# Performance work log

Measured on AMD Instinct MI355X. Metric: run time of the kernel, lower is better.

Reference implementation:

```python
import jax, jax.numpy as jnp
import numpy as np

B, S, D, H, HD = 4, 2048, 768, 12, 64
P = H * HD
LR = 0.1

def _ln(x, g, b, eps=1e-5):
    m = jnp.mean(x, axis=-1, keepdims=True)
    v = jnp.mean((x - m) ** 2, axis=-1, keepdims=True)
    return (x - m) / jnp.sqrt(v + eps) * g + b

def _modifier(x, w1, b1, w2, b2):
    # Linear -> GELU(exact) -> Linear, matching nn.Sequential(Linear, GELU, Linear)
    h = jax.nn.gelu(x @ w1.T + b1, approximate=False)
    return h @ w2.T + b2

def setup_inputs() -> dict:
    key = jax.random.key(0)
    ks = jax.random.split(key, 16)
    def n(k, shape, s=0.02):
        return jax.random.normal(k, shape, jnp.float32) * s
    inp = {}
    inp['x'] = jax.random.normal(ks[0], (B, S, D), jnp.float32)
    inp['ln_in_g'] = jnp.ones((D,), jnp.float32)
    inp['ln_in_b'] = jnp.zeros((D,), jnp.float32)
    inp['Wk'] = n(ks[1], (P, D))
    inp['Wv'] = n(ks[2], (P, D))
    inp['Wq'] = n(ks[3], (P, D))
    inp['km_w1'] = n(ks[4], (D // 4, D), 0.01); inp['km_b1'] = jnp.zeros((D // 4,), jnp.float32)
    inp['km_w2'] = n(ks[5], (P, D // 4), 0.01); inp['km_b2'] = jnp.zeros((P,), jnp.float32)
    inp['vm_w1'] = n(ks[6], (D // 4, D), 0.01); inp['vm_b1'] = jnp.zeros((D // 4,), jnp.float32)
    inp['vm_w2'] = n(ks[7], (P, D // 4), 0.01); inp['vm_b2'] = jnp.zeros((P,), jnp.float32)
    inp['qm_w1'] = n(ks[8], (D // 4, D), 0.01); inp['qm_b1'] = jnp.zeros((D // 4,), jnp.float32)
    inp['qm_w2'] = n(ks[9], (P, D // 4), 0.01); inp['qm_b2'] = jnp.zeros((P,), jnp.float32)
    inp['lnk_g'] = jnp.ones((HD,), jnp.float32); inp['lnk_b'] = jnp.zeros((HD,), jnp.float32)
    inp['lnv_g'] = jnp.ones((HD,), jnp.float32); inp['lnv_b'] = jnp.zeros((HD,), jnp.float32)
    inp['lnq_g'] = jnp.ones((HD,), jnp.float32); inp['lnq_b'] = jnp.zeros((HD,), jnp.float32)
    inp['Wo'] = n(ks[10], (D, P))
    inp['lr_scale'] = jnp.ones((H,), jnp.float32)
    inp['Wg'] = n(ks[11], (D, D))
    inp['bg'] = jnp.zeros((D,), jnp.float32)
    return inp

def reference(x, ln_in_g, ln_in_b, Wk, Wv, Wq,
              km_w1, km_b1, km_w2, km_b2,
              vm_w1, vm_b1, vm_w2, vm_b2,
              qm_w1, qm_b1, qm_w2, qm_b2,
              lnk_g, lnk_b, lnv_g, lnv_b, lnq_g, lnq_b,
              Wo, lr_scale, Wg, bg):
    b, s, d = x.shape
    xn = _ln(x, ln_in_g, ln_in_b)  # norm_input
    # data-dependent projections (context defaults to x_normed)
    k = xn @ Wk.T + 0.1 * _modifier(xn, km_w1, km_b1, km_w2, km_b2)
    v = xn @ Wv.T + 0.1 * _modifier(xn, vm_w1, vm_b1, vm_w2, vm_b2)
    q = xn @ Wq.T + 0.1 * _modifier(xn, qm_w1, qm_b1, qm_w2, qm_b2)
    k = _ln(k.reshape(b, s, H, HD), lnk_g, lnk_b)
    v = _ln(v.reshape(b, s, H, HD), lnv_g, lnv_b)
    q = _ln(q.reshape(b, s, H, HD), lnq_g, lnq_b)
    # scan over time: (s, b, h, d)
    k_s = jnp.transpose(k, (1, 0, 2, 3))
    v_s = jnp.transpose(v, (1, 0, 2, 3))
    q_s = jnp.transpose(q, (1, 0, 2, 3))
    lr = jax.nn.sigmoid(lr_scale) * LR * 2.0  # (H,)
    M0 = jnp.zeros((b, H, HD, HD), x.dtype)

    def step(M, kvq):
        k_t, v_t, q_t = kvq  # each (b, h, d)
        out_t = jnp.einsum('bhdk,bhk->bhd', M, q_t)  # read before update
        kn = k_t / (jnp.linalg.norm(k_t, axis=-1, keepdims=True) + 1e-6)
        pred = jnp.einsum('bhdk,bhk->bhd', M, kn)
        surprise = pred - v_t
        # M - outer(pred, kn) - lr * outer(surprise, kn), fused
        coef = pred + lr[None, :, None] * surprise  # (b, h, d)
        M_new = M - jnp.einsum('bhd,bhk->bhdk', coef, kn)
        return M_new, out_t

    M_final, outs = jax.lax.scan(step, M0, (k_s, v_s, q_s))  # outs: (s, b, h, d)
    out = jnp.transpose(outs, (1, 0, 2, 3)).reshape(b, s, H * HD)
    out = out @ Wo.T
    gate = jax.nn.sigmoid(x @ Wg.T + bg)  # output_gate on raw x
    out = gate * out
    return out, M_final
```

## Files before the change

kernel.cpp:

```cpp
#include <hip/hip_runtime.h>
#include <hip/hip_bf16.h>
#include <math.h>

#define B_ 4
#define S_ 2048
#define D_ 768
#define H_ 12
#define HD_ 64
#define P_ 768
#define M_ (B_*S_)
#define NCH 32
#define CH 64
#define BH (B_*H_)
#define NPAIR 16

typedef __hip_bfloat16 bf16;
typedef __attribute__((ext_vector_type(8))) short short8;
typedef __attribute__((ext_vector_type(4))) short s16x4;
typedef __attribute__((ext_vector_type(4))) float f32x4;

__device__ __forceinline__ float wave_reduce_sum(float v){
  #pragma unroll
  for (int off=32; off>0; off>>=1) v += __shfl_xor(v, off, 64);
  return v;
}
__device__ __forceinline__ float bf2f(bf16 h){ return __bfloat162float(h); }
__device__ __forceinline__ float us2f(unsigned short u){
  union{unsigned int i; float f;} z; z.i = ((unsigned int)u)<<16; return z.f;
}
__device__ __forceinline__ int adr(int row, int col){ return (row*128 + col*2) ^ ((row&7)<<4); }
__device__ __forceinline__ short8 lfrag(const char* base, int row, int col){
  return *(const short8*)(base + adr(row,col));
}
__device__ __forceinline__ short8 gfrag(const bf16* g, int row, int col){
  return *(const short8*)(g + row*64 + col);
}
__device__ __forceinline__ f32x4 MM(short8 a, short8 b, f32x4 c){
  return __builtin_amdgcn_mfma_f32_16x16x32_bf16(a, b, c, 0,0,0);
}
__device__ __forceinline__ short f2s(float v){ bf16 h = __float2bfloat16(v); return *(short*)&h; }
__device__ __forceinline__ void stpk(char* b, int n, int m0, float v0,float v1,float v2,float v3){
  s16x4 p = { f2s(v0), f2s(v1), f2s(v2), f2s(v3) };
  *(s16x4*)(b + adr(n, m0)) = p;
}
__device__ __forceinline__ void stpk_hl(char* bh, char* bl, int n, int m0,
                                        float v0,float v1,float v2,float v3){
  float h0=bf2f(__float2bfloat16(v0)), h1=bf2f(__float2bfloat16(v1));
  float h2=bf2f(__float2bfloat16(v2)), h3=bf2f(__float2bfloat16(v3));
  stpk(bh, n, m0, h0,h1,h2,h3);
  stpk(bl, n, m0, v0-h0, v1-h1, v2-h2, v3-h3);
}
__device__ __forceinline__ float4 ldpk2(const char* bh, const char* bl, int n, int m0){
  s16x4 a = *(const s16x4*)(bh + adr(n,m0));
  s16x4 b = *(const s16x4*)(bl + adr(n,m0));
  return make_float4(us2f((unsigned short)a[0])+us2f((unsigned short)b[0]),
                     us2f((unsigned short)a[1])+us2f((unsigned short)b[1]),
                     us2f((unsigned short)a[2])+us2f((unsigned short)b[2]),
                     us2f((unsigned short)a[3])+us2f((unsigned short)b[3]));
}
__device__ __forceinline__ void gl_lds(const bf16* g, const bf16* l){
  __builtin_amdgcn_global_load_lds(
      (const __attribute__((address_space(1))) void*)g,
      (__attribute__((address_space(3))) void*)l, 16, 0, 0);
}

__global__ __launch_bounds__(256) void pack_ln_kernel(
    const float* __restrict__ km1,const float* __restrict__ vm1,const float* __restrict__ qm1,
    const float* __restrict__ Wk,const float* __restrict__ Wv,const float* __restrict__ Wq,
    const float* __restrict__ k2,const float* __restrict__ v2,const float* __restrict__ q2,
    const float* __restrict__ Wo,const float* __restrict__ Wg,
    const float* __restrict__ kb1,const float* __restrict__ vb1,const float* __restrict__ qb1,
    const float* __restrict__ kb2,const float* __restrict__ vb2,const float* __restrict__ qb2,
    const float* __restrict__ lnkg,const float* __restrict__ lnvg,const float* __restrict__ lnqg,
    const float* __restrict__ lnkb,const float* __restrict__ lnvb,const float* __restrict__ lnqb,
    bf16* __restrict__ Whb, bf16* __restrict__ Wkvqb, bf16* __restrict__ Wob,
    bf16* __restrict__ Wgb, float* __restrict__ biasb,
    const float* __restrict__ x, const float* __restrict__ lng_in, const float* __restrict__ lnb_in,
    bf16* __restrict__ xn, bf16* __restrict__ xb)
{
  if (blockIdx.x >= 15181){
    int row = blockIdx.x - 15181;
    const float* xr = x + (size_t)row*D_;
    int t = threadIdx.x;
    float v0 = xr[t], v1 = xr[t+256], v2 = xr[t+512];
    float s  = v0+v1+v2;
    float sq = v0*v0+v1*v1+v2*v2;
    s = wave_reduce_sum(s); sq = wave_reduce_sum(sq);
    __shared__ float red[8];
    int w = t>>6;
    if ((t&63)==0){ red[w]=s; red[4+w]=sq; }
    __syncthreads();
    s  = red[0]+red[1]+red[2]+red[3];
    sq = red[4]+red[5]+red[6]+red[7];
    float mean = s*(1.f/D_);
    float var  = sq*(1.f/D_) - mean*mean;
    float inv  = rsqrtf(var + 1e-5f);
    bf16* xnr = xn + (size_t)row*D_;
    bf16* xbr = xb + (size_t)row*D_;
    xnr[t]     = __float2bfloat16((v0-mean)*inv*lng_in[t]     + lnb_in[t]);
    xnr[t+256] = __float2bfloat16((v1-mean)*inv*lng_in[t+256] + lnb_in[t+256]);
    xnr[t+512] = __float2bfloat16((v2-mean)*inv*lng_in[t+512] + lnb_in[t+512]);
    xbr[t] = __float2bfloat16(v0); xbr[t+256] = __float2bfloat16(v1); xbr[t+512] = __float2bfloat16(v2);
    return;
  }
  int i = blockIdx.x*256 + threadIdx.x;
  if (i < 491520){
    int r = i/768, c = i%768;
    float v = 0.f;
    if (r < 192) v = km1[r*768+c];
    else if (r < 384) v = vm1[(r-192)*768+c];
    else if (r < 576) v = qm1[(r-384)*768+c];
    Whb[i] = __float2bfloat16(v);
  } else if (i < 2703360){
    int i2 = i - 491520;
    int r = i2/960, c = i2%960;
    int p = r/768, rr = r%768;
    const float* W  = (p==0)?Wk:(p==1)?Wv:Wq;
    const float* w2 = (p==0)?k2:(p==1)?v2:q2;
    float v = (c < 768) ? W[(size_t)rr*768+c] : 0.1f*w2[(size_t)rr*192 + (c-768)];
    Wkvqb[i2] = __float2bfloat16(v);
  } else if (i < 3293184){
    int i2 = i - 2703360;
    Wob[i2] = __float2bfloat16(Wo[i2]);
  } else if (i < 3883008){
    int i2 = i - 3293184;
    Wgb[i2] = __float2bfloat16(Wg[i2]);
  } else if (i < 3886272){
    int i2 = i - 3883008;
    if (i2 < 576){
      biasb[i2] = (i2<192)? kb1[i2] : (i2<384)? vb1[i2-192] : qb1[i2-384];
    } else if (i2 < 2880){
      int r = i2-576; int p = r/768, rr = r%768;
      const float* b2 = (p==0)?kb2:(p==1)?vb2:qb2;
      biasb[i2] = 0.1f*b2[rr];
    } else if (i2 < 3072){
      int k3 = i2-2880; int gg=k3/64, cc=k3%64;
      biasb[i2] = (gg==0?lnkg:gg==1?lnvg:lnqg)[cc];
    } else {
      int k3 = i2-3072; int gg=k3/64, cc=k3%64;
      biasb[i2] = (gg==0?lnkb:gg==1?lnvb:lnqb)[cc];
    }
  }
}

template<int MODE>
__device__ __forceinline__ void gemm_core(
    const bf16* __restrict__ A1, int lda1, int K1,
    const bf16* __restrict__ A2, int lda2, int K2, int a2_gstride,
    const bf16* __restrict__ Bw, int ldb, int ngroup,
    const float* __restrict__ bias, const void* __restrict__ extra,
    const float* __restrict__ lng, const float* __restrict__ lnb,
    void* __restrict__ outp, int Nout,
    int bx, int by, int g, char* smemraw)
{
  bf16 (*Asm)[128*32] = (bf16 (*)[128*32])smemraw;
  bf16 (*Bsm)[128*32] = (bf16 (*)[128*32])(smemraw + 3*128*32*2);
  const int t = threadIdx.x;
  const int w = t>>6, L = t&63;
  const int m0 = bx*128, n0 = by*128;
  const int wm = w>>1, wn = w&1;
  const int Ktot = K1 + K2;
  const int nk = Ktot >> 5;

  const int srow = L>>2;
  const int scol8 = ((L&3) ^ ((L>>2)&3))*8;

  int aoff[4], boff[4];
  #pragma unroll
  for (int f=0;f<4;f++){
    int arow = wm*64 + f*16 + (L&15);
    int brow = wn*64 + f*16 + (L&15);
    aoff[f] = arow*32 + (((L>>4) ^ (arow&3))<<3);
    boff[f] = brow*32 + (((L>>4) ^ (brow&3))<<3);
  }

  const bf16* BrowBase = Bw + (size_t)(g*ngroup + n0)*ldb;

  auto STAGE = [&](int buf, int k0){
    const bf16* Ab; int lda; int acol;
    if (k0 < K1){ Ab = A1; lda = lda1; acol = k0 + scol8; }
    else        { Ab = A2; lda = lda2; acol = (k0-K1) + g*a2_gstride + scol8; }
    #pragma unroll
    for (int i=0;i<2;i++){
      int row = w*32 + i*16 + srow;
      gl_lds(Ab + (size_t)(m0+row)*lda + acol,         &Asm[buf][w*1024 + i*512]);
      gl_lds(BrowBase + (size_t)row*ldb + k0 + scol8,  &Bsm[buf][w*1024 + i*512]);
    }
  };

  f32x4 acc[4][4];
  #pragma unroll
  for (int i=0;i<4;i++)
    #pragma unroll
    for (int j=0;j<4;j++) acc[i][j] = (f32x4){0.f,0.f,0.f,0.f};

  STAGE(0, 0);
  STAGE(1, 32);
  int rd = 0;
  for (int kt=0; kt<nk; ++kt){
    if (kt == nk-1) asm volatile("s_waitcnt vmcnt(0)" ::: "memory");
    else            asm volatile("s_waitcnt vmcnt(4)" ::: "memory");
    asm volatile("s_waitcnt lgkmcnt(0)" ::: "memory");
    __builtin_amdgcn_s_barrier();
    __builtin_amdgcn_sched_barrier(0);
    if (kt+2 < nk){
      int st = rd+2; if (st>=3) st-=3;
      STAGE(st, (kt+2)<<5);
    }
    const bf16* As = Asm[rd];
    const bf16* Bs = Bsm[rd];
    short8 af[4], bfr[4];
    #pragma unroll
    for (int f=0;f<4;f++){
      af[f]  = *(const short8*)&As[aoff[f]];
      bfr[f] = *(const short8*)&Bs[boff[f]];
    }
    #pragma unroll
    for (int i=0;i<4;i++)
      #pragma unroll
      for (int j=0;j<4;j++)
        acc[i][j] = MM(af[i], bfr[j], acc[i][j]);
    rd = (rd==2)?0:rd+1;
  }

  if (MODE==1){
    float gco[4], bco[4];
    #pragma unroll
    for (int j=0;j<4;j++){ int cc = j*16 + (L&15); gco[j] = lng[g*64+cc]; bco[j] = lnb[g*64+cc]; }
    #pragma unroll
    for (int i=0;i<4;i++){
      #pragma unroll
      for (int r=0;r<4;r++){
        float v[4];
        #pragma unroll
        for (int j=0;j<4;j++){
          int n = n0 + wn*64 + j*16 + (L&15);
          v[j] = acc[i][j][r] + bias[g*768 + n];
        }
        float s1 = v[0]+v[1]+v[2]+v[3];
        float s2 = v[0]*v[0]+v[1]*v[1]+v[2]*v[2]+v[3]*v[3];
        #pragma unroll
        for (int mk=1; mk<16; mk<<=1){ s1 += __shfl_xor(s1, mk, 64); s2 += __shfl_xor(s2, mk, 64); }
        float mean = s1*(1.f/64.f);
        float var  = s2*(1.f/64.f) - mean*mean;
        float inv  = rsqrtf(var + 1e-5f);
        float y[4];
        #pragma unroll
        for (int j=0;j<4;j++) y[j] = (v[j]-mean)*inv*gco[j] + bco[j];
        if (g==0){
          float n2 = y[0]*y[0]+y[1]*y[1]+y[2]*y[2]+y[3]*y[3];
          #pragma unroll
          for (int mk=1; mk<16; mk<<=1) n2 += __shfl_xor(n2, mk, 64);
          float sc = 1.f/(sqrtf(n2)+1e-6f);
          #pragma unroll
          for (int j=0;j<4;j++) y[j] *= sc;
        }
        int m = m0 + wm*64 + i*16 + (L>>4)*4 + r;
        int b_ = m>>11, s_ = m&2047;
        #pragma unroll
        for (int j=0;j<4;j++){
          int n = n0 + wn*64 + j*16 + (L&15);
          int h_ = n>>6, hd = n&63;
          ((bf16*)outp)[((((size_t)g*B_ + b_)*H_ + h_)*S_ + s_)*HD_ + hd] = __float2bfloat16(y[j]);
        }
      }
    }
  } else {
    #pragma unroll
    for (int i=0;i<4;i++){
      #pragma unroll
      for (int j=0;j<4;j++){
        #pragma unroll
        for (int r=0;r<4;r++){
          int m = m0 + wm*64 + i*16 + (L>>4)*4 + r;
          int n = n0 + wn*64 + j*16 + (L&15);
          float val = acc[i][j][r];
          if (MODE==0){
            if (n < Nout){
              val += bias[n];
              float ge = 0.5f*val*(1.f + erff(val*0.70710678f));
              ((bf16*)outp)[(size_t)m*Nout + n] = __float2bfloat16(ge);
            }
          } else if (MODE==4){
            ((bf16*)outp)[(size_t)m*Nout + n] = __float2bfloat16(val);
          } else {
            float g2 = bf2f(((const bf16*)extra)[(size_t)m*768 + n]) + bias[n];
            float gate = 1.f/(1.f + __expf(-g2));
            ((float*)outp)[(size_t)m*Nout + n] = val * gate;
          }
        }
      }
    }
  }
}

template<int MODE>
__global__ __launch_bounds__(256) void gemm_kernel(
    const bf16* __restrict__ A1, int lda1, int K1,
    const bf16* __restrict__ A2, int lda2, int K2, int a2_gstride,
    const bf16* __restrict__ Bw, int ldb, int ngroup,
    const float* __restrict__ bias, const void* __restrict__ extra,
    const float* __restrict__ lng, const float* __restrict__ lnb,
    void* __restrict__ outp, int Nout)
{
  __shared__ __align__(16) char smem[49152];
  gemm_core<MODE>(A1, lda1, K1, A2, lda2, K2, a2_gstride, Bw, ldb, ngroup,
                  bias, extra, lng, lnb, outp, Nout,
                  blockIdx.x, blockIdx.y, blockIdx.z, smem);
}

__global__ __launch_bounds__(256) void prep_kernel(
    const bf16* __restrict__ kvqb, const float* __restrict__ lr_scale,
    bf16* __restrict__ WKng, bf16* __restrict__ WVTg,
    bf16* __restrict__ AcThi, bf16* __restrict__ AcTlo, bf16* __restrict__ Bcb)
{
  __shared__ __align__(16) char T1[8192];
  __shared__ __align__(16) char T2[8192];
  __shared__ __align__(16) char T3[8192];
  __shared__ __align__(16) char T4[8192];
  __shared__ __align__(16) char T5[8192];

  const int c = blockIdx.x, bh = blockIdx.y;
  const int h = bh % H_;
  const int t = threadIdx.x, w = t>>6, L = t&63;
  const size_t PS = (size_t)B_*H_*S_*HD_;
  const size_t base_k = (size_t)bh*S_*HD_ + (size_t)c*CH*HD_;
  const float lr = 0.2f/(1.f + __expf(-lr_scale[h]));
  const float beta = 1.f + lr;
  const size_t cb = ((size_t)bh*NCH + c)*4096;
  const bf16* Kg = kvqb + base_k;
  const bf16* Vg = kvqb + PS + base_k;

  const int fr = L&15, fc = (L>>4)*8;
  const int m0 = 16*w + (L>>4)*4;
  const int nb = L&15;

  {
    short8 aK[2];
    #pragma unroll
    for (int kk=0;kk<2;kk++) aK[kk] = gfrag(Kg, 16*w+fr, kk*32+fc);
    #pragma unroll
    for (int nt=0;nt<4;nt++){
      f32x4 g = (f32x4){0.f,0.f,0.f,0.f};
      #pragma unroll
      for (int kk=0;kk<2;kk++) g = MM(aK[kk], gfrag(Kg, 16*nt+fr, kk*32+fc), g);
      int n = 16*nt + nb;
      float pv[4], ptv[4], tv[4];
      #pragma unroll
      for (int r=0;r<4;r++){
        int m = m0 + r;
        float val = beta*g[r];
        pv[r]  = (n>m)? val : 0.f;
        ptv[r] = (m>n)? val : 0.f;
        tv[r]  = ((n==m)?1.f:0.f) - pv[r];
      }
      stpk(T3, n, m0, pv[0],pv[1],pv[2],pv[3]);
      stpk(T4, n, m0, ptv[0],ptv[1],ptv[2],ptv[3]);
      stpk_hl(T1, T2, n, m0, tv[0],tv[1],tv[2],tv[3]);
    }
  }
  __syncthreads();

  #pragma unroll
  for (int s=0; s<6; ++s){
    const bool do_upd = (s>=1), do_sq = (s<=4);
    f32x4 upd[4], c1[4], c2[4];
    float4 tr[4];
    short8 aPT[2];
    #pragma unroll
    for (int kk=0;kk<2;kk++) aPT[kk] = lfrag(T4, 16*w+fr, kk*32+fc);
    if (do_upd){
      short8 b1[4][2], b2[4][2];
      #pragma unroll
      for (int nt=0;nt<4;nt++){
        #pragma unroll
        for (int kk=0;kk<2;kk++){
          b1[nt][kk] = lfrag(T1, 16*nt+fr, kk*32+fc);
          b2[nt][kk] = lfrag(T2, 16*nt+fr, kk*32+fc);
        }
        upd[nt] = (f32x4){0.f,0.f,0.f,0.f};
      }
      #pragma unroll
      for (int nt=0;nt<4;nt++)
        #pragma unroll
        for (int kk=0;kk<2;kk++){
          upd[nt] = MM(aPT[kk], b1[nt][kk], upd[nt]);
          upd[nt] = MM(aPT[kk], b2[nt][kk], upd[nt]);
        }
      #pragma unroll
      for (int nt=0;nt<4;nt++) tr[nt] = ldpk2(T1, T2, 16*nt+nb, m0);
    }
    if (do_sq){
      short8 aP[2], bPT[4][2], bP[4][2];
      #pragma unroll
      for (int kk=0;kk<2;kk++) aP[kk] = lfrag(T3, 16*w+fr, kk*32+fc);
      #pragma unroll
      for (int nt=0;nt<4;nt++){
        #pragma unroll
        for (int kk=0;kk<2;kk++){
          bPT[nt][kk] = lfrag(T4, 16*nt+fr, kk*32+fc);
          bP[nt][kk]  = lfrag(T3, 16*nt+fr, kk*32+fc);
        }
        c1[nt] = (f32x4){0.f,0.f,0.f,0.f};
        c2[nt] = (f32x4){0.f,0.f,0.f,0.f};
      }
      #pragma unroll
      for (int nt=0;nt<4;nt++)
        #pragma unroll
        for (int kk=0;kk<2;kk++){
          c1[nt] = MM(aP[kk],  bPT[nt][kk], c1[nt]);
          c2[nt] = MM(aPT[kk], bP[nt][kk],  c2[nt]);
        }
    }
    __syncthreads();
    if (do_upd){
      #pragma unroll
      for (int nt=0;nt<4;nt++){
        int n = 16*nt + nb;
        stpk_hl(T1, T2, n, m0, tr[nt].x+upd[nt][0], tr[nt].y+upd[nt][1],
                               tr[nt].z+upd[nt][2], tr[nt].w+upd[nt][3]);
      }
    }
    if (do_sq){
      #pragma unroll
      for (int nt=0;nt<4;nt++){
        int n = 16*nt + nb;
        stpk(T4, n, m0, c1[nt][0],c1[nt][1],c1[nt][2],c1[nt][3]);
        stpk(T3, n, m0, c2[nt][0],c2[nt][1],c2[nt][2],c2[nt][3]);
      }
    }
    __syncthreads();
  }

  {
    short8 aKg[2], aVg[2];
    #pragma unroll
    for (int kk=0;kk<2;kk++){
      aKg[kk] = gfrag(Kg, 16*w+fr, kk*32+fc);
      aVg[kk] = gfrag(Vg, 16*w+fr, kk*32+fc);
    }
    #pragma unroll
    for (int nt=0;nt<4;nt++){
      f32x4 ck = (f32x4){0.f,0.f,0.f,0.f};
      f32x4 cv = (f32x4){0.f,0.f,0.f,0.f};
      int row = 16*nt + nb;
      #pragma unroll
      for (int kk=0;kk<2;kk++){
        short8 bi;
        int col0 = kk*32 + fc;
        #pragma unroll
        for (int e=0;e<8;e++) bi[e] = (col0+e == 16*nt+fr) ? (short)0x3F80 : (short)0;
        ck = MM(aKg[kk], bi, ck);
        cv = MM(aVg[kk], bi, cv);
      }
      stpk(T3, row, m0, ck[0],ck[1],ck[2],ck[3]);
      stpk(T4, row, m0, cv[0],cv[1],cv[2],cv[3]);
    }
  }
  __syncthreads();

  {
    short8 a1[2], a2[2];
    #pragma unroll
    for (int kk=0;kk<2;kk++){
      a1[kk] = lfrag(T1, 16*w+fr, kk*32+fc);
      a2[kk] = lfrag(T2, 16*w+fr, kk*32+fc);
    }
    f32x4 cwv[4], cwk[4];
    #pragma unroll
    for (int nt=0;nt<4;nt++){ cwv[nt]=(f32x4){0.f,0.f,0.f,0.f}; cwk[nt]=(f32x4){0.f,0.f,0.f,0.f}; }
    #pragma unroll
    for (int nt=0;nt<4;nt++)
      #pragma unroll
      for (int kk=0;kk<2;kk++){
        short8 bV = lfrag(T4, 16*nt+fr, kk*32+fc);
        cwv[nt] = MM(a1[kk], bV, cwv[nt]);
        cwv[nt] = MM(a2[kk], bV, cwv[nt]);
      }
    #pragma unroll
    for (int nt=0;nt<4;nt++)
      #pragma unroll
      for (int kk=0;kk<2;kk++){
        short8 bK = lfrag(T3, 16*nt+fr, kk*32+fc);
        cwk[nt] = MM(a1[kk], bK, cwk[nt]);
        cwk[nt] = MM(a2[kk], bK, cwk[nt]);
      }
    __syncthreads();
    #pragma unroll
    for (int nt=0;nt<4;nt++){
      int n = 16*nt + nb;
      stpk(T5, n, m0, cwv[nt][0],cwv[nt][1],cwv[nt][2],cwv[nt][3]);
      stpk(T4, n, m0, cwk[nt][0],cwk[nt][1],cwk[nt][2],cwk[nt][3]);
    }
  }
  __syncthreads();

  {
    int row = t>>2, seg = (t&3)*16;
    size_t go = cb + (size_t)row*64 + seg;
    *(short8*)(WVTg+go)   = *(const short8*)(T5 + adr(row,seg));
    *(short8*)(WVTg+go+8) = *(const short8*)(T5 + adr(row,seg+8));

    short8 aK2[2], aWKT[2];
    #pragma unroll
    for (int kk=0;kk<2;kk++){
      aK2[kk]  = lfrag(T3, 16*w+fr, kk*32+fc);
      aWKT[kk] = lfrag(T4, 16*w+fr, kk*32+fc);
    }
    f32x4 cBc[4], cWK[4], cAc[4];
    #pragma unroll
    for (int nt=0;nt<4;nt++){ cBc[nt]=(f32x4){0.f,0.f,0.f,0.f}; cWK[nt]=(f32x4){0.f,0.f,0.f,0.f}; cAc[nt]=(f32x4){0.f,0.f,0.f,0.f}; }
    #pragma unroll
    for (int nt=0;nt<4;nt++)
      #pragma unroll
      for (int kk=0;kk<2;kk++){
        short8 bWVT = lfrag(T5, 16*nt+fr, kk*32+fc);
        cBc[nt] = MM(aK2[kk], bWVT, cBc[nt]);
      }
    #pragma unroll
    for (int nt=0;nt<4;nt++)
      #pragma unroll
      for (int kk=0;kk<2;kk++){
        short8 b1 = lfrag(T1, 16*nt+fr, kk*32+fc);
        short8 b2 = lfrag(T2, 16*nt+fr, kk*32+fc);
        cWK[nt] = MM(aK2[kk], b1, cWK[nt]);
        cWK[nt] = MM(aK2[kk], b2, cWK[nt]);
      }
    #pragma unroll
    for (int nt=0;nt<4;nt++)
      #pragma unroll
      for (int kk=0;kk<2;kk++){
        short8 bK3 = lfrag(T3, 16*nt+fr, kk*32+fc);
        cAc[nt] = MM(aWKT[kk], bK3, cAc[nt]);
      }
    __syncthreads();
    #pragma unroll
    for (int nt=0;nt<4;nt++){
      int n = 16*nt + nb;
      stpk(T5, n, m0, lr*cBc[nt][0], lr*cBc[nt][1], lr*cBc[nt][2], lr*cBc[nt][3]);
      stpk(T3, n, m0, cWK[nt][0],cWK[nt][1],cWK[nt][2],cWK[nt][3]);
      float av[4];
      #pragma unroll
      for (int r=0;r<4;r++) av[r] = ((n==m0+r)?1.f:0.f) - beta*cAc[nt][r];
      stpk_hl(T1, T2, n, m0, av[0],av[1],av[2],av[3]);
    }
  }
  __syncthreads();

  {
    int row = t>>2, seg = (t&3)*16;
    size_t go = cb + (size_t)row*64 + seg;
    *(short8*)(AcThi+go)   = *(const short8*)(T1 + adr(row,seg));
    *(short8*)(AcThi+go+8) = *(const short8*)(T1 + adr(row,seg+8));
    *(short8*)(AcTlo+go)   = *(const short8*)(T2 + adr(row,seg));
    *(short8*)(AcTlo+go+8) = *(const short8*)(T2 + adr(row,seg+8));
    *(short8*)(Bcb+go)     = *(const short8*)(T5 + adr(row,seg));
    *(short8*)(Bcb+go+8)   = *(const short8*)(T5 + adr(row,seg+8));
    *(short8*)(WKng+go)    = *(const short8*)(T3 + adr(row,seg));
    *(short8*)(WKng+go+8)  = *(const short8*)(T3 + adr(row,seg+8));
  }
}

__global__ __launch_bounds__(256) void prep2_kernel(
    const bf16* __restrict__ AcThi, const bf16* __restrict__ AcTlo, const bf16* __restrict__ Bcb,
    bf16* __restrict__ A2h, bf16* __restrict__ A2l,
    bf16* __restrict__ BT2h, bf16* __restrict__ BT2l)
{
  __shared__ __align__(16) char TA[8192];
  __shared__ __align__(16) char TB[8192];
  const int i = blockIdx.x, bh = blockIdx.y;
  const int t = threadIdx.x, w = t>>6, L = t&63;
  const size_t cb0 = ((size_t)bh*NCH + 2*i)*4096;
  const size_t cb1 = cb0 + 4096;
  const size_t pb  = ((size_t)bh*NPAIR + i)*4096;
  const int fr = L&15, fc = (L>>4)*8;
  const int m0 = 16*w + (L>>4)*4;
  const int nb = L&15;

  {
    short8 s0[2], s1[2];
    #pragma unroll
    for (int kk=0;kk<2;kk++){
      s0[kk] = *(const short8*)(AcThi + cb0 + (size_t)(16*w+fr)*64 + kk*32 + fc);
      s1[kk] = *(const short8*)(AcTlo + cb0 + (size_t)(16*w+fr)*64 + kk*32 + fc);
    }
    #pragma unroll
    for (int nt=0;nt<4;nt++){
      f32x4 c0v={0.f,0.f,0.f,0.f}, c1v={0.f,0.f,0.f,0.f};
      #pragma unroll
      for (int kk=0;kk<2;kk++){
        short8 bi;
        int col0 = kk*32 + fc;
        #pragma unroll
        for (int e=0;e<8;e++) bi[e] = (col0+e == 16*nt+fr) ? (short)0x3F80 : (short)0;
        c0v = MM(s0[kk], bi, c0v);
        c1v = MM(s1[kk], bi, c1v);
      }
      stpk(TA, 16*nt+nb, m0, c0v[0],c0v[1],c0v[2],c0v[3]);
      stpk(TB, 16*nt+nb, m0, c1v[0],c1v[1],c1v[2],c1v[3]);
    }
  }
  __syncthreads();
  {
    short8 aTh[2], aTl[2], gAh[2], gAl[2];
    #pragma unroll
    for (int kk=0;kk<2;kk++){
      aTh[kk] = lfrag(TA, 16*w+fr, kk*32+fc);
      aTl[kk] = lfrag(TB, 16*w+fr, kk*32+fc);
      gAh[kk] = *(const short8*)(AcThi + cb1 + (size_t)(16*w+fr)*64 + kk*32 + fc);
      gAl[kk] = *(const short8*)(AcTlo + cb1 + (size_t)(16*w+fr)*64 + kk*32 + fc);
    }
    #pragma unroll
    for (int nt=0;nt<4;nt++){
      short8 gBh[2], gBl[2], bB0[2];
      #pragma unroll
      for (int kk=0;kk<2;kk++){
        gBh[kk] = *(const short8*)(AcThi + cb1 + (size_t)(16*nt+fr)*64 + kk*32 + fc);
        gBl[kk] = *(const short8*)(AcTlo + cb1 + (size_t)(16*nt+fr)*64 + kk*32 + fc);
        bB0[kk] = *(const short8*)(Bcb   + cb0 + (size_t)(16*nt+fr)*64 + kk*32 + fc);
      }
      f32x4 accA = {0.f,0.f,0.f,0.f};
      s16x4 b1pk = *(const s16x4*)(Bcb + cb1 + (size_t)(16*nt+nb)*64 + m0);
      f32x4 accB = { us2f((unsigned short)b1pk[0]), us2f((unsigned short)b1pk[1]),
                     us2f((unsigned short)b1pk[2]), us2f((unsigned short)b1pk[3]) };
      #pragma unroll
      for (int kk=0;kk<2;kk++){
        accA = MM(aTh[kk], gBh[kk], accA);
        accA = MM(aTl[kk], gBh[kk], accA);
        accA = MM(aTh[kk], gBl[kk], accA);
        accB = MM(gAh[kk], bB0[kk], accB);
        accB = MM(gAl[kk], bB0[kk], accB);
      }
      int n = 16*nt + nb;
      size_t go = pb + (size_t)n*64 + m0;
      float h0[4], l0[4], h1[4], l1[4];
      #pragma unroll
      for (int r=0;r<4;r++){
        h0[r] = bf2f(__float2bfloat16(accA[r])); l0[r] = accA[r]-h0[r];
        h1[r] = bf2f(__float2bfloat16(accB[r])); l1[r] = accB[r]-h1[r];
      }
      s16x4 pa = { f2s(h0[0]), f2s(h0[1]), f2s(h0[2]), f2s(h0[3]) };
      s16x4 pbv= { f2s(l0[0]), f2s(l0[1]), f2s(l0[2]), f2s(l0[3]) };
      s16x4 pc = { f2s(h1[0]), f2s(h1[1]), f2s(h1[2]), f2s(h1[3]) };
      s16x4 pd = { f2s(l1[0]), f2s(l1[1]), f2s(l1[2]), f2s(l1[3]) };
      *(s16x4*)(A2h  + go) = pa;
      *(s16x4*)(A2l  + go) = pbv;
      *(s16x4*)(BT2h + go) = pc;
      *(s16x4*)(BT2l + go) = pd;
    }
  }
}

__global__ __launch_bounds__(256) void seq_kernel(
    const bf16* __restrict__ AcThi, const bf16* __restrict__ AcTlo, const bf16* __restrict__ Bcb,
    const bf16* __restrict__ A2h, const bf16* __restrict__ A2l,
    const bf16* __restrict__ BT2h, const bf16* __restrict__ BT2l,
    bf16* __restrict__ Mpref, bf16* __restrict__ Mplo, float* __restrict__ Mout,
    const bf16* __restrict__ xb, const bf16* __restrict__ Wgb, bf16* __restrict__ G2b)
{
  __shared__ __align__(16) char smem[49152];
  if (blockIdx.x >= BH){
    int bidx = blockIdx.x - BH;
    gemm_core<4>(xb, 768, 768, nullptr, 0, 0, 0, Wgb, 768, 768,
                 nullptr, nullptr, nullptr, nullptr, G2b, 768,
                 bidx & 63, bidx >> 6, 0, smem);
    return;
  }
  char* sH0 = smem;           char* sH1 = smem + 8192;
  char* sL0 = smem + 16384;   char* sL1 = smem + 24576;
  const int bh = blockIdx.x;
  const int t = threadIdx.x, w = t>>6, L = t&63;
  const size_t cbase = (size_t)bh*NCH*4096;
  const size_t pbase = (size_t)bh*NPAIR*4096;
  const int fr = L&15, fc = (L>>4)*8;
  const int nb = L&15, cmr = (L>>4)*4;
  const int m0 = 16*w + cmr;

  { float4 z = {0.f,0.f,0.f,0.f};
    ((float4*)sH0)[t] = z; ((float4*)sH0)[t+256] = z;
    ((float4*)sL0)[t] = z; ((float4*)sL0)[t+256] = z;
    short8 zs = {0,0,0,0,0,0,0,0};
    ((short8*)(Mpref + cbase))[t] = zs; ((short8*)(Mpref + cbase))[t+256] = zs;
    ((short8*)(Mplo  + cbase))[t] = zs; ((short8*)(Mplo  + cbase))[t+256] = zs;
  }

  short8 A2hf[2], A2lf[2], Achf[2], Aclf[2];
  auto loadA = [&](int i){
    size_t pb  = pbase + (size_t)i*4096;
    size_t cb0 = cbase + (size_t)(2*i)*4096;
    #pragma unroll
    for (int kk=0;kk<2;kk++){
      size_t o = (size_t)(16*w+fr)*64 + kk*32 + fc;
      A2hf[kk] = *(const short8*)(A2h + pb + o);
      A2lf[kk] = *(const short8*)(A2l + pb + o);
      Achf[kk] = *(const short8*)(AcThi + cb0 + o);
      Aclf[kk] = *(const short8*)(AcTlo + cb0 + o);
    }
  };
  loadA(0);
  char *rh = sH0, *rl = sL0, *wh = sH1, *wl = sL1;

  for (int i=0; i<NPAIR; ++i){
    size_t pb  = pbase + (size_t)i*4096;
    size_t cb0 = cbase + (size_t)(2*i)*4096;
    asm volatile("s_waitcnt lgkmcnt(0)" ::: "memory");
    __builtin_amdgcn_s_barrier();
    __builtin_amdgcn_sched_barrier(0);
    #pragma unroll
    for (int nt=0;nt<4;nt++){
      short8 bMh[2], bMl[2];
      #pragma unroll
      for (int kk=0;kk<2;kk++){
        bMh[kk] = lfrag(rh, 16*nt+fr, kk*32+fc);
        bMl[kk] = lfrag(rl, 16*nt+fr, kk*32+fc);
      }
      f32x4 ae = {0.f,0.f,0.f,0.f}, ao = {0.f,0.f,0.f,0.f};
      #pragma unroll
      for (int kk=0;kk<2;kk++){
        ae = MM(A2hf[kk], bMh[kk], ae);
        ae = MM(A2hf[kk], bMl[kk], ae);
        ae = MM(A2lf[kk], bMh[kk], ae);
        ao = MM(Achf[kk], bMh[kk], ao);
        ao = MM(Achf[kk], bMl[kk], ao);
        ao = MM(Aclf[kk], bMh[kk], ao);
      }
      int d = 16*nt + nb;
      size_t off = (size_t)d*64 + m0;
      s16x4 b2h = *(const s16x4*)(BT2h + pb + off);
      s16x4 b2l = *(const s16x4*)(BT2l + pb + off);
      s16x4 b0  = *(const s16x4*)(Bcb  + cb0 + off);
      float e[4], o[4];
      #pragma unroll
      for (int r=0;r<4;r++){
        e[r] = ae[r] + us2f((unsigned short)b2h[r]) + us2f((unsigned short)b2l[r]);
        o[r] = ao[r] + us2f((unsigned short)b0[r]);
      }
      {
        float h[4], lo[4];
        #pragma unroll
        for (int r=0;r<4;r++){ h[r] = bf2f(__float2bfloat16(o[r])); lo[r] = o[r]-h[r]; }
        size_t go = cbase + (size_t)(2*i+1)*4096 + off;
        s16x4 ph = { f2s(h[0]), f2s(h[1]), f2s(h[2]), f2s(h[3]) };
        s16x4 pl = { f2s(lo[0]), f2s(lo[1]), f2s(lo[2]), f2s(lo[3]) };
        *(s16x4*)(Mpref + go) = ph;
        *(s16x4*)(Mplo  + go) = pl;
      }
      {
        float h[4], lo[4];
        #pragma unroll
        for (int r=0;r<4;r++){ h[r] = bf2f(__float2bfloat16(e[r])); lo[r] = e[r]-h[r]; }
        stpk(wh, d, m0, h[0],h[1],h[2],h[3]);
        stpk(wl, d, m0, lo[0],lo[1],lo[2],lo[3]);
        if (i < NPAIR-1){
          size_t go = cbase + (size_t)(2*i+2)*4096 + off;
          s16x4 ph = { f2s(h[0]), f2s(h[1]), f2s(h[2]), f2s(h[3]) };
          s16x4 pl = { f2s(lo[0]), f2s(lo[1]), f2s(lo[2]), f2s(lo[3]) };
          *(s16x4*)(Mpref + go) = ph;
          *(s16x4*)(Mplo  + go) = pl;
        } else {
          float4 fv = { e[0], e[1], e[2], e[3] };
          *(float4*)(Mout + ((size_t)bh*64 + d)*64 + m0) = fv;
        }
      }
    }
    if (i+1 < NPAIR) loadA(i+1);
    char* tmp;
    tmp = rh; rh = wh; wh = tmp;
    tmp = rl; rl = wl; wl = tmp;
  }
}

__global__ __launch_bounds__(256) void outphase_kernel(
    const bf16* __restrict__ kvqb, const bf16* __restrict__ Mpref, const bf16* __restrict__ Mplo,
    const bf16* __restrict__ WKng, const bf16* __restrict__ WVTb,
    const float* __restrict__ lr_scale, bf16* __restrict__ attn)
{
  __shared__ __align__(16) char sUT[8192];
  __shared__ __align__(16) char sAT[8192];
  const int c = blockIdx.x, bh = blockIdx.y;
  const int b = bh / H_, h = bh % H_;
  const int t = threadIdx.x, w = t>>6, L = t&63;
  const size_t PS = (size_t)B_*H_*S_*HD_;
  const size_t cb = ((size_t)bh*NCH + c)*4096;
  const size_t base_k = (size_t)bh*S_*HD_ + (size_t)c*CH*HD_;
  const bf16* Kg = kvqb + base_k;
  const bf16* Qg = kvqb + 2*PS + base_k;
  const float lr = 0.2f/(1.f + __expf(-lr_scale[h]));
  const float beta = 1.f + lr;
  const int fr = L&15, fc = (L>>4)*8;
  const int m0 = 16*w + (L>>4)*4;
  const int nb = L&15;

  {
    short8 aKn[2];
    #pragma unroll
    for (int kk=0;kk<2;kk++) aKn[kk] = gfrag(Kg, 16*w+fr, kk*32+fc);
    #pragma unroll
    for (int nt=0;nt<4;nt++){
      f32x4 cat = (f32x4){0.f,0.f,0.f,0.f};
      #pragma unroll
      for (int kk=0;kk<2;kk++) cat = MM(aKn[kk], gfrag(Qg, 16*nt+fr, kk*32+fc), cat);
      int n = 16*nt + nb;
      float v[4];
      #pragma unroll
      for (int r=0;r<4;r++) v[r] = (m0+r < n)? cat[r] : 0.f;
      stpk(sAT, n, m0, v[0],v[1],v[2],v[3]);
    }
  }

  short8 mbh[4][2], mbl[4][2], qa[2], wa[2];
  #pragma unroll
  for (int kk=0;kk<2;kk++){
    qa[kk] = gfrag(Qg, 16*w+fr, kk*32+fc);
    wa[kk] = *(const short8*)(WKng + cb + (size_t)(16*w + fr)*64 + kk*32 + fc);
  }
  #pragma unroll
  for (int nt=0;nt<4;nt++)
    #pragma unroll
    for (int kk=0;kk<2;kk++){
      size_t o = cb + (size_t)(16*nt + fr)*64 + kk*32 + fc;
      mbh[nt][kk] = *(const short8*)(Mpref + o);
      mbl[nt][kk] = *(const short8*)(Mplo  + o);
    }
  f32x4 aout[4], ap[4];
  #pragma unroll
  for (int nt=0;nt<4;nt++){ aout[nt]=(f32x4){0.f,0.f,0.f,0.f}; ap[nt]=(f32x4){0.f,0.f,0.f,0.f}; }
  #pragma unroll
  for (int nt=0;nt<4;nt++)
    #pragma unroll
    for (int kk=0;kk<2;kk++){
      aout[nt] = MM(qa[kk], mbh[nt][kk], aout[nt]);
      aout[nt] = MM(qa[kk], mbl[nt][kk], aout[nt]);
      ap[nt]   = MM(wa[kk], mbh[nt][kk], ap[nt]);
      ap[nt]   = MM(wa[kk], mbl[nt][kk], ap[nt]);
    }
  #pragma unroll
  for (int nt=0;nt<4;nt++){
    s16x4 wv4 = *(const s16x4*)(WVTb + cb + (size_t)(nt*16 + (L&15))*64 + 16*w + (L>>4)*4);
    short us[4];
    #pragma unroll
    for (int r=0;r<4;r++){
      float wv = us2f((unsigned short)wv4[r]);
      us[r] = f2s(lr*wv - beta*ap[nt][r]);
    }
    int d = nt*16 + (L&15);
    int i0 = 16*w + (L>>4)*4;
    s16x4 pk = { us[0], us[1], us[2], us[3] };
    *(s16x4*)(sUT + adr(d, i0)) = pk;
  }
  __syncthreads();
  short8 ta[2], ub[4][2];
  #pragma unroll
  for (int kk=0;kk<2;kk++)
    ta[kk] = lfrag(sAT, 16*w+fr, kk*32+fc);
  #pragma unroll
  for (int nt=0;nt<4;nt++)
    #pragma unroll
    for (int kk=0;kk<2;kk++)
      ub[nt][kk] = lfrag(sUT, 16*nt + fr, kk*32 + fc);
  #pragma unroll
  for (int nt=0;nt<4;nt++)
    #pragma unroll
    for (int kk=0;kk<2;kk++)
      aout[nt] = MM(ta[kk], ub[nt][kk], aout[nt]);
  #pragma unroll
  for (int nt=0;nt<4;nt++)
    #pragma unroll
    for (int r=0;r<4;r++)
      attn[((size_t)b*S_ + (size_t)c*CH + 16*w + (L>>4)*4 + r)*P_ + h*HD_ + nt*16 + (L&15)]
        = __float2bfloat16(aout[nt][r]);
}

extern "C" void kernel_launch(void* const* d_in, const int* in_sizes, int n_in,
                              void* d_out, int out_size, void* d_ws, size_t ws_size,
                              hipStream_t stream)
{
  const float* x     = (const float*)d_in[0];
  const float* ln_g  = (const float*)d_in[1];
  const float* ln_b  = (const float*)d_in[2];
  const float* Wk    = (const float*)d_in[3];
  const float* Wv    = (const float*)d_in[4];
  const float* Wq    = (const float*)d_in[5];
  const float* km_w1 = (const float*)d_in[6];  const float* km_b1 = (const float*)d_in[7];
  const float* km_w2 = (const float*)d_in[8];  const float* km_b2 = (const float*)d_in[9];
  const float* vm_w1 = (const float*)d_in[10]; const float* vm_b1 = (const float*)d_in[11];
  const float* vm_w2 = (const float*)d_in[12]; const float* vm_b2 = (const float*)d_in[13];
  const float* qm_w1 = (const float*)d_in[14]; const float* qm_b1 = (const float*)d_in[15];
  const float* qm_w2 = (const float*)d_in[16]; const float* qm_b2 = (const float*)d_in[17];
  const float* lnk_g = (const float*)d_in[18]; const float* lnk_b = (const float*)d_in[19];
  const float* lnv_g = (const float*)d_in[20]; const float* lnv_b = (const float*)d_in[21];
  const float* lnq_g = (const float*)d_in[22]; const float* lnq_b = (const float*)d_in[23];
  const float* Wo    = (const float*)d_in[24];
  const float* lr_sc = (const float*)d_in[25];
  const float* Wg    = (const float*)d_in[26];
  const float* bg    = (const float*)d_in[27];

  const size_t CHB = (size_t)BH*NCH*4096;
  const size_t PRB = (size_t)BH*NPAIR*4096;

  char* ws = (char*)d_ws;
  size_t o = 0;
  bf16* xnb   = (bf16*)(ws + o); o += (size_t)M_*D_*2;
  bf16* xb    = (bf16*)(ws + o); o += (size_t)M_*D_*2;
  bf16* Hb    = (bf16*)(ws + o); o += (size_t)M_*576*2;
  bf16* kvqb  = (bf16*)(ws + o); o += (size_t)3*M_*P_*2;
  bf16* attn  = (bf16*)(ws + o); o += (size_t)M_*P_*2;
  bf16* AcThi = (bf16*)(ws + o); o += CHB*2;
  bf16* AcTlo = (bf16*)(ws + o); o += CHB*2;
  bf16* Bcb   = (bf16*)(ws + o); o += CHB*2;
  bf16* WVTb  = (bf16*)(ws + o); o += CHB*2;
  bf16* WKng  = (bf16*)(ws + o); o += CHB*2;
  bf16* Mpref = (bf16*)(ws + o); o += CHB*2;
  bf16* Mplo  = (bf16*)(ws + o); o += CHB*2;
  bf16* A2h   = (bf16*)(ws + o); o += PRB*2;
  bf16* A2l   = (bf16*)(ws + o); o += PRB*2;
  bf16* BT2h  = (bf16*)(ws + o); o += PRB*2;
  bf16* BT2l  = (bf16*)(ws + o); o += PRB*2;
  bf16* Whb   = (bf16*)(ws + o); o += (size_t)640*768*2;
  bf16* Wkvqb = (bf16*)(ws + o); o += (size_t)2304*960*2;
  bf16* Wob   = (bf16*)(ws + o); o += (size_t)768*768*2;
  bf16* Wgb   = (bf16*)(ws + o); o += (size_t)768*768*2;
  float* biasb= (float*)(ws + o); o += 3264*4;
  bf16* G2b   = xnb;

  float* outF = (float*)d_out;
  float* Mout = outF + (size_t)M_*D_;

  pack_ln_kernel<<<15181 + M_, 256, 0, stream>>>(
      km_w1, vm_w1, qm_w1, Wk, Wv, Wq, km_w2, vm_w2, qm_w2, Wo, Wg,
      km_b1, vm_b1, qm_b1, km_b2, vm_b2, qm_b2,
      lnk_g, lnv_g, lnq_g, lnk_b, lnv_b, lnq_b,
      Whb, Wkvqb, Wob, Wgb, biasb,
      x, ln_g, ln_b, xnb, xb);

  gemm_kernel<0><<<dim3(64,5,1), 256, 0, stream>>>(xnb, 768, 768, nullptr, 0, 0, 0,
                                                   Whb, 768, 640, biasb, nullptr, nullptr, nullptr, Hb, 576);
  gemm_kernel<1><<<dim3(64,6,3), 256, 0, stream>>>(xnb, 768, 768, Hb, 576, 192, 192,
                                                   Wkvqb, 960, 768, biasb + 576, nullptr,
                                                   biasb + 2880, biasb + 3072, kvqb, 768);

  prep_kernel<<<dim3(NCH, BH), 256, 0, stream>>>(kvqb, lr_sc, WKng, WVTb, AcThi, AcTlo, Bcb);
  prep2_kernel<<<dim3(NPAIR, BH), 256, 0, stream>>>(AcThi, AcTlo, Bcb, A2h, A2l, BT2h, BT2l);

  seq_kernel<<<BH + 384, 256, 0, stream>>>(AcThi, AcTlo, Bcb, A2h, A2l, BT2h, BT2l,
                                           Mpref, Mplo, Mout, xb, Wgb, G2b);

  outphase_kernel<<<dim3(NCH, BH), 256, 0, stream>>>(kvqb, Mpref, Mplo, WKng, WVTb, lr_sc, attn);

  gemm_kernel<3><<<dim3(64,6,1), 256, 0, stream>>>(attn, 768, 768, nullptr, 0, 0, 0,
                                                   Wob, 768, 768, bg, G2b, nullptr, nullptr, outF, 768);
}
```

Baseline: 269.2 us.

## Split seq_kernel chain work across two wave groups with 512-thread blocks

The sequential memory-state kernel now runs 512 threads per block, with one group of four waves computing the pair-step state update and another computing the odd-chunk prefix output. Each wave issues half the MFMAs per step, which shortens the serial critical path of the recurrence. The side gate GEMM blocks are replaced by a dedicated 256x128-tile routine sized for 512 threads, halving their block count. This raises per-block register and thread pressure and changes co-scheduling between the recurrence blocks and the gate GEMM blocks.

```diff
diff --git a/kernel.cpp b/kernel.cpp
--- a/kernel.cpp
+++ b/kernel.cpp
@@ -281,8 +281,6 @@
               float ge = 0.5f*val*(1.f + erff(val*0.70710678f));
               ((bf16*)outp)[(size_t)m*Nout + n] = __float2bfloat16(ge);
             }
-          } else if (MODE==4){
-            ((bf16*)outp)[(size_t)m*Nout + n] = __float2bfloat16(val);
           } else {
             float g2 = bf2f(((const bf16*)extra)[(size_t)m*768 + n]) + bias[n];
             float gate = 1.f/(1.f + __expf(-g2));
@@ -307,6 +305,79 @@
   gemm_core<MODE>(A1, lda1, K1, A2, lda2, K2, a2_gstride, Bw, ldb, ngroup,
                   bias, extra, lng, lnb, outp, Nout,
                   blockIdx.x, blockIdx.y, blockIdx.z, smem);
+}
+
+__device__ __forceinline__ void g2_512(
+    const bf16* __restrict__ xb, const bf16* __restrict__ Wgb, bf16* __restrict__ G2b,
+    int bx, int by, char* smemraw)
+{
+  bf16 (*Asm)[256*32] = (bf16 (*)[256*32])smemraw;
+  bf16 (*Bsm)[128*32] = (bf16 (*)[128*32])(smemraw + 2*256*32*2);
+  const int t = threadIdx.x;
+  const int w = t>>6, L = t&63;
+  const int m0 = bx*256, n0 = by*128;
+  const int wm = w>>1, wn = w&1;
+
+  const int srow = L>>2;
+  const int scol8 = ((L&3) ^ ((L>>2)&3))*8;
+
+  int aoff[4], boff[4];
+  #pragma unroll
+  for (int f=0;f<4;f++){
+    int arow = wm*64 + f*16 + (L&15);
+    int brow = wn*64 + f*16 + (L&15);
+    aoff[f] = arow*32 + (((L>>4) ^ (arow&3))<<3);
+    boff[f] = brow*32 + (((L>>4) ^ (brow&3))<<3);
+  }
+
+  auto STAGE = [&](int buf, int k0){
+    #pragma unroll
+    for (int i=0;i<2;i++){
+      int row = w*32 + i*16 + srow;
+      gl_lds(xb + (size_t)(m0+row)*768 + k0 + scol8, &Asm[buf][w*1024 + i*512]);
+    }
+    int brow = w*16 + srow;
+    gl_lds(Wgb + (size_t)(n0+brow)*768 + k0 + scol8, &Bsm[buf][w*512]);
+  };
+
+  f32x4 acc[4][4];
+  #pragma unroll
+  for (int i=0;i<4;i++)
+    #pragma unroll
+    for (int j=0;j<4;j++) acc[i][j] = (f32x4){0.f,0.f,0.f,0.f};
+
+  STAGE(0, 0);
+  int cur = 0;
+  for (int kt=0; kt<24; ++kt){
+    asm volatile("s_waitcnt vmcnt(0)" ::: "memory");
+    __syncthreads();
+    if (kt+1 < 24) STAGE(cur^1, (kt+1)<<5);
+    const bf16* As = Asm[cur];
+    const bf16* Bs = Bsm[cur];
+    short8 af[4], bfr[4];
+    #pragma unroll
+    for (int f=0;f<4;f++){
+      af[f]  = *(const short8*)&As[aoff[f]];
+      bfr[f] = *(const short8*)&Bs[boff[f]];
+    }
+    #pragma unroll
+    for (int i=0;i<4;i++)
+      #pragma unroll
+      for (int j=0;j<4;j++)
+        acc[i][j] = MM(af[i], bfr[j], acc[i][j]);
+    cur ^= 1;
+  }
+
+  #pragma unroll
+  for (int i=0;i<4;i++)
+    #pragma unroll
+    for (int j=0;j<4;j++)
+      #pragma unroll
+      for (int r=0;r<4;r++){
+        int m = m0 + wm*64 + i*16 + (L>>4)*4 + r;
+        int n = n0 + wn*64 + j*16 + (L&15);
+        G2b[(size_t)m*768 + n] = __float2bfloat16(acc[i][j][r]);
+      }
 }
 
 __global__ __launch_bounds__(256) void prep_kernel(
@@ -651,7 +722,7 @@
   }
 }
 
-__global__ __launch_bounds__(256) void seq_kernel(
+__global__ __launch_bounds__(512) void seq_kernel(
     const bf16* __restrict__ AcThi, const bf16* __restrict__ AcTlo, const bf16* __restrict__ Bcb,
     const bf16* __restrict__ A2h, const bf16* __restrict__ A2l,
     const bf16* __restrict__ BT2h, const bf16* __restrict__ BT2l,
@@ -661,40 +732,40 @@
   __shared__ __align__(16) char smem[49152];
   if (blockIdx.x >= BH){
     int bidx = blockIdx.x - BH;
-    gemm_core<4>(xb, 768, 768, nullptr, 0, 0, 0, Wgb, 768, 768,
-                 nullptr, nullptr, nullptr, nullptr, G2b, 768,
-                 bidx & 63, bidx >> 6, 0, smem);
+    g2_512(xb, Wgb, G2b, bidx & 31, bidx >> 5, smem);
     return;
   }
   char* sH0 = smem;           char* sH1 = smem + 8192;
   char* sL0 = smem + 16384;   char* sL1 = smem + 24576;
   const int bh = blockIdx.x;
   const int t = threadIdx.x, w = t>>6, L = t&63;
+  const int grp = w>>2;
+  const int jw  = w&3;
   const size_t cbase = (size_t)bh*NCH*4096;
   const size_t pbase = (size_t)bh*NPAIR*4096;
   const int fr = L&15, fc = (L>>4)*8;
   const int nb = L&15, cmr = (L>>4)*4;
-  const int m0 = 16*w + cmr;
+  const int m0 = 16*jw + cmr;
 
   { float4 z = {0.f,0.f,0.f,0.f};
-    ((float4*)sH0)[t] = z; ((float4*)sH0)[t+256] = z;
-    ((float4*)sL0)[t] = z; ((float4*)sL0)[t+256] = z;
+    ((float4*)sH0)[t] = z;
+    ((float4*)sL0)[t] = z;
     short8 zs = {0,0,0,0,0,0,0,0};
-    ((short8*)(Mpref + cbase))[t] = zs; ((short8*)(Mpref + cbase))[t+256] = zs;
-    ((short8*)(Mplo  + cbase))[t] = zs; ((short8*)(Mplo  + cbase))[t+256] = zs;
-  }
-
-  short8 A2hf[2], A2lf[2], Achf[2], Aclf[2];
+    ((short8*)(Mpref + cbase))[t] = zs;
+    ((short8*)(Mplo  + cbase))[t] = zs;
+  }
+
+  const bf16* Ah_src = grp ? AcThi : A2h;
+  const bf16* Al_src = grp ? AcTlo : A2l;
+
+  short8 Ahf[2], Alf[2];
   auto loadA = [&](int i){
-    size_t pb  = pbase + (size_t)i*4096;
-    size_t cb0 = cbase + (size_t)(2*i)*4096;
+    size_t ab = grp ? (cbase + (size_t)(2*i)*4096) : (pbase + (size_t)i*4096);
     #pragma unroll
     for (int kk=0;kk<2;kk++){
-      size_t o = (size_t)(16*w+fr)*64 + kk*32 + fc;
-      A2hf[kk] = *(const short8*)(A2h + pb + o);
-      A2lf[kk] = *(const short8*)(A2l + pb + o);
-      Achf[kk] = *(const short8*)(AcThi + cb0 + o);
-      Aclf[kk] = *(const short8*)(AcTlo + cb0 + o);
+      size_t o = ab + (size_t)(16*jw+fr)*64 + kk*32 + fc;
+      Ahf[kk] = *(const short8*)(Ah_src + o);
+      Alf[kk] = *(const short8*)(Al_src + o);
     }
   };
   loadA(0);
@@ -714,41 +785,25 @@
         bMh[kk] = lfrag(rh, 16*nt+fr, kk*32+fc);
         bMl[kk] = lfrag(rl, 16*nt+fr, kk*32+fc);
       }
-      f32x4 ae = {0.f,0.f,0.f,0.f}, ao = {0.f,0.f,0.f,0.f};
+      f32x4 a = {0.f,0.f,0.f,0.f};
       #pragma unroll
       for (int kk=0;kk<2;kk++){
-        ae = MM(A2hf[kk], bMh[kk], ae);
-        ae = MM(A2hf[kk], bMl[kk], ae);
-        ae = MM(A2lf[kk], bMh[kk], ae);
-        ao = MM(Achf[kk], bMh[kk], ao);
-        ao = MM(Achf[kk], bMl[kk], ao);
-        ao = MM(Aclf[kk], bMh[kk], ao);
+        a = MM(Ahf[kk], bMh[kk], a);
+        a = MM(Ahf[kk], bMl[kk], a);
+        a = MM(Alf[kk], bMh[kk], a);
       }
       int d = 16*nt + nb;
       size_t off = (size_t)d*64 + m0;
-      s16x4 b2h = *(const s16x4*)(BT2h + pb + off);
-      s16x4 b2l = *(const s16x4*)(BT2l + pb + off);
-      s16x4 b0  = *(const s16x4*)(Bcb  + cb0 + off);
-      float e[4], o[4];
-      #pragma unroll
-      for (int r=0;r<4;r++){
-        e[r] = ae[r] + us2f((unsigned short)b2h[r]) + us2f((unsigned short)b2l[r]);
-        o[r] = ao[r] + us2f((unsigned short)b0[r]);
-      }
-      {
+      float v[4];
+      if (grp == 0){
+        s16x4 b2h = *(const s16x4*)(BT2h + pb + off);
+        s16x4 b2l = *(const s16x4*)(BT2l + pb + off);
+        #pragma unroll
+        for (int r=0;r<4;r++)
+          v[r] = a[r] + us2f((unsigned short)b2h[r]) + us2f((unsigned short)b2l[r]);
         float h[4], lo[4];
         #pragma unroll
-        for (int r=0;r<4;r++){ h[r] = bf2f(__float2bfloat16(o[r])); lo[r] = o[r]-h[r]; }
-        size_t go = cbase + (size_t)(2*i+1)*4096 + off;
-        s16x4 ph = { f2s(h[0]), f2s(h[1]), f2s(h[2]), f2s(h[3]) };
-        s16x4 pl = { f2s(lo[0]), f2s(lo[1]), f2s(lo[2]), f2s(lo[3]) };
-        *(s16x4*)(Mpref + go) = ph;
-        *(s16x4*)(Mplo  + go) = pl;
-      }
-      {
-        float h[4], lo[4];
-        #pragma unroll
-        for (int r=0;r<4;r++){ h[r] = bf2f(__float2bfloat16(e[r])); lo[r] = e[r]-h[r]; }
+        for (int r=0;r<4;r++){ h[r] = bf2f(__float2bfloat16(v[r])); lo[r] = v[r]-h[r]; }
         stpk(wh, d, m0, h[0],h[1],h[2],h[3]);
         stpk(wl, d, m0, lo[0],lo[1],lo[2],lo[3]);
         if (i < NPAIR-1){
@@ -758,9 +813,22 @@
           *(s16x4*)(Mpref + go) = ph;
           *(s16x4*)(Mplo  + go) = pl;
         } else {
-          float4 fv = { e[0], e[1], e[2], e[3] };
+          float4 fv = { v[0], v[1], v[2], v[3] };
           *(float4*)(Mout + ((size_t)bh*64 + d)*64 + m0) = fv;
         }
+      } else {
+        s16x4 b0 = *(const s16x4*)(Bcb + cb0 + off);
+        #pragma unroll
+        for (int r=0;r<4;r++)
+          v[r] = a[r] + us2f((unsigned short)b0[r]);
+        float h[4], lo[4];
+        #pragma unroll
+        for (int r=0;r<4;r++){ h[r] = bf2f(__float2bfloat16(v[r])); lo[r] = v[r]-h[r]; }
+        size_t go = cbase + (size_t)(2*i+1)*4096 + off;
+        s16x4 ph = { f2s(h[0]), f2s(h[1]), f2s(h[2]), f2s(h[3]) };
+        s16x4 pl = { f2s(lo[0]), f2s(lo[1]), f2s(lo[2]), f2s(lo[3]) };
+        *(s16x4*)(Mpref + go) = ph;
+        *(s16x4*)(Mplo  + go) = pl;
       }
     }
     if (i+1 < NPAIR) loadA(i+1);
@@ -942,7 +1010,7 @@
   prep_kernel<<<dim3(NCH, BH), 256, 0, stream>>>(kvqb, lr_sc, WKng, WVTb, AcThi, AcTlo, Bcb);
   prep2_kernel<<<dim3(NPAIR, BH), 256, 0, stream>>>(AcThi, AcTlo, Bcb, A2h, A2l, BT2h, BT2l);
 
-  seq_kernel<<<BH + 384, 256, 0, stream>>>(AcThi, AcTlo, Bcb, A2h, A2l, BT2h, BT2l,
+  seq_kernel<<<BH + 192, 512, 0, stream>>>(AcThi, AcTlo, Bcb, A2h, A2l, BT2h, BT2l,
                                            Mpref, Mplo, Mout, xb, Wgb, G2b);
 
   outphase_kernel<<<dim3(NCH, BH), 256, 0, stream>>>(kvqb, Mpref, Mplo, WKng, WVTb, lr_sc, attn);
```

After: 264.1 us. Within noise of the previous version (-1.9%).
